# Performance work log

Hardware: AMD Instinct MI355X
Metric: run time of the kernel (lower is better)

The kernel has to match this reference:

```python
import jax, jax.numpy as jnp
import numpy as np

NUM_HEADS = 8
SCALE = 25.0
SIM_THRESH = 0.75


def setup_inputs() -> dict:
    key = jax.random.key(0)
    k1, k2, k3, k4 = jax.random.split(key, 4)
    B, N, C = 1, 2048, 1024
    x_cls = jax.random.normal(k1, (B, N, C), jnp.float32)
    cls_score = jax.random.uniform(k2, (N,), jnp.float32)
    fg_score = jax.random.uniform(k3, (N,), jnp.float32)
    W_qkv = jax.random.normal(k4, (3 * C, C), jnp.float32) * 0.02
    return {"x_cls": x_cls, "cls_score": cls_score, "fg_score": fg_score, "W_qkv": W_qkv}


def reference(x_cls, cls_score, fg_score, W_qkv):
    B, N, C = x_cls.shape
    H = NUM_HEADS
    hd = C // H
    # qkv projection (Linear without bias): [B,N,3C] -> [3,B,H,N,hd]
    qkv = (x_cls @ W_qkv.T).reshape(B, N, 3, H, hd).transpose(2, 0, 3, 1, 4)
    q, k, v = qkv[0], qkv[1], qkv[2]
    # cosine normalization
    qn = q / jnp.linalg.norm(q, axis=-1, keepdims=True)
    kn = k / jnp.linalg.norm(k, axis=-1, keepdims=True)
    vn = v / jnp.linalg.norm(v, axis=-1, keepdims=True)
    # cls_score broadcast to [1,1,1,N] (columns); fg_score is unused downstream
    cs = cls_score.reshape(1, 1, 1, N)
    # raw v-v similarity map [B,H,N,N]
    attn_cls_raw = vn @ jnp.swapaxes(vn, -2, -1)
    # use_mask=True path: mask[i,j] = cls_score[j] > cls_score[i] - 0.1
    cs_mask = (cs > jnp.swapaxes(cs, -2, -1) - 0.1).astype(x_cls.dtype)
    # scaled, score-weighted, masked attention; dropout p=0 is identity
    attn = jax.nn.softmax((qn @ jnp.swapaxes(kn, -2, -1)) * SCALE * cs * cs_mask, axis=-1)
    x = jnp.swapaxes(attn @ v, 1, 2).reshape(B, N, C)
    x_ori = jnp.swapaxes(v, 1, 2).reshape(B, N, C)
    x_out = jnp.concatenate([x, x_ori], axis=-1)  # [B,N,2C]
    # ave=True branch: head-averaged similarity + second softmax, masked renorm
    sim_raw = attn_cls_raw.sum(axis=1)[0] / H  # [N,N]
    sim_mask = (sim_raw > SIM_THRESH).astype(x_cls.dtype)
    sim_attn = attn.sum(axis=1)[0] / H
    sim_round2 = jax.nn.softmax(sim_attn, axis=-1)
    masked = sim_mask * sim_round2
    sim_round2 = masked / jnp.sum(masked, axis=-1, keepdims=True)
    return (x_out, sim_round2)
```

## Files before the change

### kernel.cpp

```cpp
#include <hip/hip_runtime.h>
#include <cstdint>

typedef unsigned short u16;
typedef __attribute__((ext_vector_type(8))) short short8;
typedef __attribute__((ext_vector_type(4))) short short4v;
typedef __attribute__((ext_vector_type(4))) float f32x4;

#define NTOK 2048
#define CDIM 1024
#define C3   3072
#define NH   8
#define HD   128

__device__ __forceinline__ float bf2f(u16 u) {
    return __uint_as_float(((unsigned)u) << 16);
}
__device__ __forceinline__ u16 f2bf(float f) {
    unsigned u = __float_as_uint(f);
    u += 0x7fffu + ((u >> 16) & 1u);
    return (u16)(u >> 16);
}
__device__ __forceinline__ void gld_lds16(const u16* g, u16* l) {
    __builtin_amdgcn_global_load_lds(
        (__attribute__((address_space(1))) void*)(u16*)g,
        (__attribute__((address_space(3))) void*)l, 16, 0, 0);
}

__global__ __launch_bounds__(256) void k_cast(const float* __restrict__ x,
                                              const float* __restrict__ w,
                                              u16* __restrict__ xb,
                                              u16* __restrict__ wb) {
    int t = blockIdx.x * blockDim.x + threadIdx.x;
    int stride = gridDim.x * blockDim.x;
    for (int i = t; i < (NTOK * CDIM) / 4; i += stride) {
        float4 v = ((const float4*)x)[i];
        ushort4 o;
        o.x = f2bf(v.x); o.y = f2bf(v.y); o.z = f2bf(v.z); o.w = f2bf(v.w);
        ((ushort4*)xb)[i] = o;
    }
    for (int i = t; i < (C3 * CDIM) / 4; i += stride) {
        float4 v = ((const float4*)w)[i];
        ushort4 o;
        o.x = f2bf(v.x); o.y = f2bf(v.y); o.z = f2bf(v.z); o.w = f2bf(v.w);
        ((ushort4*)wb)[i] = o;
    }
}

__global__ __launch_bounds__(256) void k_qkvn(const u16* __restrict__ A,
                                              const u16* __restrict__ B,
                                              u16* __restrict__ Qn,
                                              u16* __restrict__ Kn,
                                              u16* __restrict__ Vn,
                                              u16* __restrict__ Vt,
                                              float* __restrict__ out) {
    __shared__ u16 SB[2][16384];
    __shared__ float rowssq[128][2];
    u16* T = (u16*)SB;
    const int tid = threadIdx.x;
    const int lane = tid & 63;
    const int wid = tid >> 6;
    const int wm = wid >> 1, wn = wid & 1;
    const int q = lane >> 4, l16 = lane & 15;
    const int s = blockIdx.x;
    const int which = s >> 3, h = s & 7;
    const int m0 = blockIdx.y * 128, n0 = s * 128;

    const u16* aP[4];
    const u16* bP[4];
#pragma unroll
    for (int t = 0; t < 4; t++) {
        int sl = tid + t * 256;
        int r = sl >> 3, c = (sl & 7) * 8;
        aP[t] = &A[(long long)(m0 + r) * CDIM + c];
        bP[t] = &B[(long long)(n0 + r) * CDIM + c];
    }
#pragma unroll
    for (int t = 0; t < 4; t++) {
        int sl = tid + t * 256;
        gld_lds16(aP[t], &SB[0][sl * 8]);
        gld_lds16(bP[t], &SB[0][8192 + sl * 8]);
        aP[t] += 64;
        bP[t] += 64;
    }

    f32x4 zero4 = {0.f, 0.f, 0.f, 0.f};
    f32x4 acc[4][4];
#pragma unroll
    for (int i = 0; i < 4; i++)
#pragma unroll
        for (int j = 0; j < 4; j++) acc[i][j] = zero4;

    for (int jt = 0; jt < 16; ++jt) {
        const u16* As = SB[jt & 1];
        const u16* Bs = SB[jt & 1] + 8192;
        asm volatile("s_waitcnt vmcnt(0)" ::: "memory");
        __builtin_amdgcn_s_barrier();
        asm volatile("" ::: "memory");
        if (jt < 15) {
            u16* Sx = SB[(jt + 1) & 1];
#pragma unroll
            for (int t = 0; t < 4; t++) {
                int sl = tid + t * 256;
                gld_lds16(aP[t], &Sx[sl * 8]);
                gld_lds16(bP[t], &Sx[8192 + sl * 8]);
                aP[t] += 64;
                bP[t] += 64;
            }
        }
#pragma unroll
        for (int ks = 0; ks < 2; ks++) {
            short8 af[4], bfr[4];
#pragma unroll
            for (int tm = 0; tm < 4; tm++)
                af[tm] = *(const short8*)&As[(wm * 64 + tm * 16 + l16) * 64 + ks * 32 + q * 8];
#pragma unroll
            for (int tn = 0; tn < 4; tn++)
                bfr[tn] = *(const short8*)&Bs[(wn * 64 + tn * 16 + l16) * 64 + ks * 32 + q * 8];
#pragma unroll
            for (int tm = 0; tm < 4; tm++)
#pragma unroll
                for (int tn = 0; tn < 4; tn++)
                    acc[tm][tn] = __builtin_amdgcn_mfma_f32_16x16x32_bf16(
                        af[tm], bfr[tn], acc[tm][tn], 0, 0, 0);
        }
    }

    __syncthreads();
#pragma unroll
    for (int tm = 0; tm < 4; tm++)
#pragma unroll
        for (int r = 0; r < 4; r++) {
            float p = 0.f;
#pragma unroll
            for (int tn = 0; tn < 4; tn++) p += acc[tm][tn][r] * acc[tm][tn][r];
            p += __shfl_xor(p, 1);
            p += __shfl_xor(p, 2);
            p += __shfl_xor(p, 4);
            p += __shfl_xor(p, 8);
            if (l16 == 0) rowssq[wm * 64 + tm * 16 + q * 4 + r][wn] = p;
        }
    __syncthreads();
    float rinv[4][4];
#pragma unroll
    for (int tm = 0; tm < 4; tm++)
#pragma unroll
        for (int r = 0; r < 4; r++) {
            int rl = wm * 64 + tm * 16 + q * 4 + r;
            rinv[tm][r] = rsqrtf(rowssq[rl][0] + rowssq[rl][1]);
        }
    u16* dstBase = (which == 0 ? Qn : which == 1 ? Kn : Vn);
#pragma unroll
    for (int tm = 0; tm < 4; tm++)
#pragma unroll
        for (int tn = 0; tn < 4; tn++)
#pragma unroll
            for (int r = 0; r < 4; r++) {
                int rl = wm * 64 + tm * 16 + q * 4 + r;
                int d = wn * 64 + tn * 16 + l16;
                dstBase[(long long)(m0 + rl) * CDIM + h * HD + d] =
                    f2bf(acc[tm][tn][r] * rinv[tm][r]);
            }
    if (which == 2) {
#pragma unroll
        for (int tm = 0; tm < 4; tm++)
#pragma unroll
            for (int tn = 0; tn < 4; tn++)
#pragma unroll
                for (int r = 0; r < 4; r++) {
                    int rl = wm * 64 + tm * 16 + q * 4 + r;
                    int d = wn * 64 + tn * 16 + l16;
                    float v = acc[tm][tn][r];
                    out[(long long)(m0 + rl) * 2048 + 1024 + h * HD + d] = v;
                    T[rl * 136 + d] = f2bf(v);
                }
        __syncthreads();
#pragma unroll
        for (int p = 0; p < 2; p++) {
            int drow = p * 64 + (tid >> 2);
            int nc = (tid & 3) * 32;
            u16 buf[32];
#pragma unroll
            for (int i = 0; i < 32; i++) buf[i] = T[(nc + i) * 136 + drow];
            u16* dst = &Vt[(long long)(h * HD + drow) * NTOK + m0 + nc];
            *(short8*)&dst[0] = *(short8*)&buf[0];
            *(short8*)&dst[8] = *(short8*)&buf[8];
            *(short8*)&dst[16] = *(short8*)&buf[16];
            *(short8*)&dst[24] = *(short8*)&buf[24];
        }
    }
}

__global__ __launch_bounds__(256) void k_gemm_mask(const u16* __restrict__ A,
                                                   const u16* __restrict__ B,
                                                   unsigned char* __restrict__ Cv,
                                                   int K, int lda, int ldb, int ldc,
                                                   float scale) {
    __shared__ u16 As2[2][8192];
    __shared__ u16 Bs2[2][4096];
    __shared__ __attribute__((aligned(16))) unsigned char Tm[128][80];
    const int tid = threadIdx.x;
    const int lane = tid & 63;
    const int wid = tid >> 6;
    const int wm = wid >> 1, wn = wid & 1;
    const int q = lane >> 4, l16 = lane & 15;
    const int bid = blockIdx.x + 32 * blockIdx.y;
    const int sw = (bid & 7) * 64 + (bid >> 3);
    const int m0 = (sw >> 5) * 128, n0 = (sw & 31) * 64;

    const u16* aP[4];
    const u16* bP[2];
#pragma unroll
    for (int t = 0; t < 4; t++) {
        int s = tid + t * 256;
        aP[t] = &A[(long long)(m0 + (s >> 3)) * lda + (s & 7) * 8];
    }
#pragma unroll
    for (int t = 0; t < 2; t++) {
        int s = tid + t * 256;
        bP[t] = &B[(long long)(n0 + (s >> 3)) * ldb + (s & 7) * 8];
    }
#pragma unroll
    for (int t = 0; t < 4; t++) { gld_lds16(aP[t], &As2[0][(tid + t * 256) * 8]); aP[t] += 64; }
#pragma unroll
    for (int t = 0; t < 2; t++) { gld_lds16(bP[t], &Bs2[0][(tid + t * 256) * 8]); bP[t] += 64; }

    f32x4 zero4 = {0.f, 0.f, 0.f, 0.f};
    f32x4 acc[4][2];
#pragma unroll
    for (int i = 0; i < 4; i++)
#pragma unroll
        for (int j = 0; j < 2; j++) acc[i][j] = zero4;

    const int NIT = K / 64;
    for (int jt = 0; jt < NIT; ++jt) {
        const u16* As = As2[jt & 1];
        const u16* Bs = Bs2[jt & 1];
        asm volatile("s_waitcnt vmcnt(0)" ::: "memory");
        __builtin_amdgcn_s_barrier();
        asm volatile("" ::: "memory");
        if (jt < NIT - 1) {
            u16* Ax = As2[(jt + 1) & 1];
            u16* Bx = Bs2[(jt + 1) & 1];
#pragma unroll
            for (int t = 0; t < 4; t++) { gld_lds16(aP[t], &Ax[(tid + t * 256) * 8]); aP[t] += 64; }
#pragma unroll
            for (int t = 0; t < 2; t++) { gld_lds16(bP[t], &Bx[(tid + t * 256) * 8]); bP[t] += 64; }
        }
#pragma unroll
        for (int ks = 0; ks < 2; ks++) {
            short8 af[4], bfr[2];
#pragma unroll
            for (int tm = 0; tm < 4; tm++)
                af[tm] = *(const short8*)&As[(wm * 64 + tm * 16 + l16) * 64 + ks * 32 + q * 8];
#pragma unroll
            for (int tn = 0; tn < 2; tn++)
                bfr[tn] = *(const short8*)&Bs[(wn * 32 + tn * 16 + l16) * 64 + ks * 32 + q * 8];
#pragma unroll
            for (int tm = 0; tm < 4; tm++)
#pragma unroll
                for (int tn = 0; tn < 2; tn++)
                    acc[tm][tn] = __builtin_amdgcn_mfma_f32_16x16x32_bf16(
                        af[tm], bfr[tn], acc[tm][tn], 0, 0, 0);
        }
    }

#pragma unroll
    for (int tm = 0; tm < 4; tm++)
#pragma unroll
        for (int tn = 0; tn < 2; tn++) {
            int col = wn * 32 + tn * 16 + l16;
            int rowbase = wm * 64 + tm * 16 + q * 4;
#pragma unroll
            for (int r = 0; r < 4; r++)
                Tm[rowbase + r][col] = (acc[tm][tn][r] * scale > 0.75f) ? 1 : 0;
        }
    __syncthreads();
    {
        int row = tid >> 1, half = (tid & 1) * 32;
        const short8* sm = (const short8*)&Tm[row][half];
        short8* dm = (short8*)&Cv[(long long)(m0 + row) * ldc + n0 + half];
        dm[0] = sm[0]; dm[1] = sm[1];
    }
}

__global__ __launch_bounds__(256, 2) void k_attn9(const u16* __restrict__ Qn,
                                                  const u16* __restrict__ Kn,
                                                  const u16* __restrict__ Vt,
                                                  const float* __restrict__ cls,
                                                  u16* __restrict__ P,
                                                  float* __restrict__ Spart,
                                                  u16* __restrict__ Xpart) {
    __shared__ u16 Kf[2][8192];
    __shared__ u16 Vf[2][8192];
    __shared__ u16 Et[8192];
    const int bid = blockIdx.x + 16 * (blockIdx.y + 4 * blockIdx.z);
    const int sw = (bid & 7) * 64 + (bid >> 3);
    const int h = sw >> 6;
    const int jc = (sw >> 4) & 3;
    const int i0 = (sw & 15) * 128;
    const int jbase = jc * 512;
    const int tid = threadIdx.x, lane = tid & 63, wid = tid >> 6;
    const int q = lane >> 4, l16 = lane & 15;
    const int wm = wid >> 1, wn = wid & 1;

    short8 af[4][4];
#pragma unroll
    for (int m = 0; m < 4; m++)
#pragma unroll
        for (int kt = 0; kt < 4; kt++)
            af[m][kt] = *(const short8*)&Qn[(long long)(i0 + wm * 64 + m * 16 + l16) * CDIM +
                                            h * HD + kt * 32 + q * 8];
    float cls_i[4][4];
#pragma unroll
    for (int m = 0; m < 4; m++)
#pragma unroll
        for (int r = 0; r < 4; r++)
            cls_i[m][r] = cls[i0 + wm * 64 + m * 16 + q * 4 + r] - 0.1f;

    const u16* ksrc[4];
    const u16* vsrc[4];
#pragma unroll
    for (int t = 0; t < 4; t++) {
        int g = wid * 4 + t;
        int tn = g >> 2, kt = g & 3;
        ksrc[t] = &Kn[(long long)(jbase + tn * 16 + l16) * CDIM + h * HD + kt * 32 + q * 8];
        int n = g >> 1, ks = g & 1;
        vsrc[t] = &Vt[(long long)(h * HD + n * 16 + l16) * NTOK + jbase + (ks * 4 + q) * 8];
    }

    f32x4 zero4 = {0.f, 0.f, 0.f, 0.f};
    f32x4 pv[4][4];
#pragma unroll
    for (int m = 0; m < 4; m++)
#pragma unroll
        for (int n = 0; n < 4; n++) pv[m][n] = zero4;
    float sums[4][4];
#pragma unroll
    for (int m = 0; m < 4; m++)
#pragma unroll
        for (int r = 0; r < 4; r++) sums[m][r] = 0.f;

#pragma unroll
    for (int t = 0; t < 4; t++) {
        int g = wid * 4 + t;
        gld_lds16(ksrc[t], &Kf[0][(g * 64 + lane) * 8]);
        gld_lds16(vsrc[t], &Vf[0][(g * 64 + lane) * 8]);
        ksrc[t] += 64 * CDIM;
        vsrc[t] += 64;
    }

    for (int jt = 0; jt < 8; ++jt) {
        const int j0 = jbase + jt * 64;
        const int cur = jt & 1;
        u16* Kc = Kf[cur];
        if (jt == 0)
            asm volatile("s_waitcnt vmcnt(0)" ::: "memory");
        else
            asm volatile("s_waitcnt vmcnt(4)" ::: "memory");
        float cjv[2];
        cjv[0] = cls[j0 + (wn * 2 + 0) * 16 + l16];
        cjv[1] = cls[j0 + (wn * 2 + 1) * 16 + l16];
        asm volatile("" ::: "memory");
        __builtin_amdgcn_s_barrier();
        asm volatile("" ::: "memory");
        if (jt < 7) {
            u16* Kx = Kf[cur ^ 1];
            u16* Vx = Vf[cur ^ 1];
#pragma unroll
            for (int t = 0; t < 4; t++) {
                int g = wid * 4 + t;
                gld_lds16(ksrc[t], &Kx[(g * 64 + lane) * 8]);
                gld_lds16(vsrc[t], &Vx[(g * 64 + lane) * 8]);
                ksrc[t] += 64 * CDIM;
                vsrc[t] += 64;
            }
        }
#pragma unroll
        for (int tn = 0; tn < 2; tn++) {
            int tng = wn * 2 + tn;
            short8 bfr[4];
#pragma unroll
            for (int kt = 0; kt < 4; kt++)
                bfr[kt] = *(const short8*)&Kc[((tng * 4 + kt) * 64 + lane) * 8];
            float cj = cjv[tn];
            float sc = 25.f * cj;
#pragma unroll
            for (int m = 0; m < 4; m++) {
                f32x4 acc = zero4;
                __builtin_amdgcn_s_setprio(1);
#pragma unroll
                for (int kt = 0; kt < 4; kt++)
                    acc = __builtin_amdgcn_mfma_f32_16x16x32_bf16(af[m][kt], bfr[kt],
                                                                  acc, 0, 0, 0);
                __builtin_amdgcn_s_setprio(0);
                int ibase = wm * 64 + m * 16 + q * 4;
#pragma unroll
                for (int r = 0; r < 4; r++) {
                    float mk = (cj > cls_i[m][r]) ? 1.f : 0.f;
                    float e = __expf(acc[r] * sc * mk);
                    sums[m][r] += e;
                    int il = ibase + r;
                    int jl = tng * 16 + l16;
                    Et[il * 64 + ((((jl >> 3) ^ (il & 7)) << 3) | (jl & 7))] = f2bf(e);
                }
            }
        }
        asm volatile("s_waitcnt lgkmcnt(0)" ::: "memory");
        __builtin_amdgcn_s_barrier();
        asm volatile("" ::: "memory");
        {
            int il = tid >> 1, c4 = (tid & 1) * 4;
            int x = il & 7;
            short8 e0 = *(const short8*)&Et[il * 64 + (((c4 + 0) ^ x) << 3)];
            short8 e1 = *(const short8*)&Et[il * 64 + (((c4 + 1) ^ x) << 3)];
            short8 e2 = *(const short8*)&Et[il * 64 + (((c4 + 2) ^ x) << 3)];
            short8 e3 = *(const short8*)&Et[il * 64 + (((c4 + 3) ^ x) << 3)];
            u16* dst = &P[((long long)(h * NTOK + i0 + il)) * NTOK + j0 + c4 * 8];
            *(short8*)&dst[0] = e0;
            *(short8*)&dst[8] = e1;
            *(short8*)&dst[16] = e2;
            *(short8*)&dst[24] = e3;
        }
        __builtin_amdgcn_s_setprio(1);
#pragma unroll
        for (int ks = 0; ks < 2; ks++) {
            short8 a2[4];
#pragma unroll
            for (int m2 = 0; m2 < 4; m2++) {
                int il = wm * 64 + m2 * 16 + l16;
                int ch = ks * 4 + q;
                a2[m2] = *(const short8*)&Et[il * 64 + ((ch ^ (il & 7)) << 3)];
            }
#pragma unroll
            for (int n2 = 0; n2 < 4; n2++) {
                short8 b2 = *(const short8*)&Vf[cur][(((wn * 4 + n2) * 2 + ks) * 64 + lane) * 8];
#pragma unroll
                for (int m2 = 0; m2 < 4; m2++)
                    pv[m2][n2] = __builtin_amdgcn_mfma_f32_16x16x32_bf16(
                        a2[m2], b2, pv[m2][n2], 0, 0, 0);
            }
        }
        __builtin_amdgcn_s_setprio(0);
    }
#pragma unroll
    for (int m = 0; m < 4; m++)
#pragma unroll
        for (int r = 0; r < 4; r++) {
            float s = sums[m][r];
            s += __shfl_xor(s, 1);
            s += __shfl_xor(s, 2);
            s += __shfl_xor(s, 4);
            s += __shfl_xor(s, 8);
            if (l16 == 0)
                Spart[((wn * 4 + jc) * NH + h) * NTOK + i0 + wm * 64 + m * 16 + q * 4 + r] = s;
        }
    u16* Xp = Xpart + (long long)jc * NTOK * CDIM;
#pragma unroll
    for (int m2 = 0; m2 < 4; m2++)
#pragma unroll
        for (int n2 = 0; n2 < 4; n2++)
#pragma unroll
            for (int r = 0; r < 4; r++) {
                int i = i0 + wm * 64 + m2 * 16 + q * 4 + r;
                int d = wn * 64 + n2 * 16 + l16;
                Xp[(long long)i * CDIM + h * HD + d] = f2bf(pv[m2][n2][r]);
            }
}

__global__ __launch_bounds__(256) void k_epi(const u16* __restrict__ Xpart,
                                             const float* __restrict__ Spart,
                                             const u16* __restrict__ P,
                                             const unsigned char* __restrict__ mask,
                                             float* __restrict__ out,
                                             float* __restrict__ out2) {
    __shared__ float red[256];
    __shared__ float sArr[NH];
    const int i = blockIdx.x;
    const int t = threadIdx.x;
    if (t < NH) {
        float s = 0.f;
#pragma unroll
        for (int g = 0; g < 8; g++) s += Spart[(g * NH + t) * NTOK + i];
        sArr[t] = s;
    }
    __syncthreads();
    {
        int c = t * 4;
        int h = c >> 7;
        float acc[4] = {0.f, 0.f, 0.f, 0.f};
#pragma unroll
        for (int jc = 0; jc < 4; jc++) {
            short4v v = *(const short4v*)&Xpart[(long long)jc * NTOK * CDIM +
                                                (long long)i * CDIM + c];
#pragma unroll
            for (int k = 0; k < 4; k++) acc[k] += bf2f((u16)v[k]);
        }
        float invs = 1.f / sArr[h];
        float4 o;
        o.x = acc[0] * invs; o.y = acc[1] * invs; o.z = acc[2] * invs; o.w = acc[3] * invs;
        *(float4*)&out[(long long)i * 2048 + c] = o;
    }
    float invS[NH];
#pragma unroll
    for (int h = 0; h < NH; h++) invS[h] = 1.f / (8.f * sArr[h]);
    const int c0 = t * 8;
    float a[8] = {0.f, 0.f, 0.f, 0.f, 0.f, 0.f, 0.f, 0.f};
#pragma unroll
    for (int h = 0; h < NH; h++) {
        short8 p = *(const short8*)&P[((long long)h * NTOK + i) * NTOK + c0];
#pragma unroll
        for (int k = 0; k < 8; k++) a[k] += bf2f((u16)p[k]) * invS[h];
    }
    const unsigned char* mrow = mask + (long long)i * NTOK + c0;
    float e[8];
    unsigned char mk[8];
    float part = 0.f;
#pragma unroll
    for (int k = 0; k < 8; k++) {
        e[k] = __expf(a[k]);
        mk[k] = mrow[k];
        if (mk[k]) part += e[k];
    }
    red[t] = part;
    __syncthreads();
    for (int s = 128; s > 0; s >>= 1) {
        if (t < s) red[t] += red[t + s];
        __syncthreads();
    }
    float invT = 1.f / red[0];
    float o[8];
#pragma unroll
    for (int k = 0; k < 8; k++) o[k] = mk[k] ? e[k] * invT : 0.f;
    float4 o0, o1;
    o0.x = o[0]; o0.y = o[1]; o0.z = o[2]; o0.w = o[3];
    o1.x = o[4]; o1.y = o[5]; o1.z = o[6]; o1.w = o[7];
    float* dst = out2 + (long long)i * NTOK + c0;
    *(float4*)dst = o0;
    *(float4*)(dst + 4) = o1;
}

extern "C" void kernel_launch(void* const* d_in, const int* in_sizes, int n_in,
                              void* d_out, int out_size, void* d_ws,
                              size_t ws_size, hipStream_t stream) {
    (void)in_sizes; (void)n_in; (void)out_size; (void)ws_size;
    const float* x = (const float*)d_in[0];
    const float* cls = (const float*)d_in[1];
    const float* Wq = (const float*)d_in[3];
    float* out = (float*)d_out;
    char* ws = (char*)d_ws;

    u16* Xb = (u16*)(ws + 0);
    u16* Wb = (u16*)(ws + 4194304);
    u16* Xpart = (u16*)(ws + 0);
    float* Spart = (float*)(ws + 16777216);
    u16* Qn = (u16*)(ws + 23068672);
    u16* Kn = (u16*)(ws + 27262976);
    u16* Vn = (u16*)(ws + 31457280);
    u16* Vt = (u16*)(ws + 35651584);
    unsigned char* mask = (unsigned char*)(ws + 39845888);
    u16* P = (u16*)(ws + 44040192);

    k_cast<<<1024, 256, 0, stream>>>(x, Wq, Xb, Wb);

    k_qkvn<<<dim3(24, 16), 256, 0, stream>>>(Xb, Wb, Qn, Kn, Vn, Vt, out);

    k_gemm_mask<<<dim3(32, 16), 256, 0, stream>>>(
        Vn, Vn, mask, CDIM, CDIM, CDIM, NTOK, 0.125f);

    k_attn9<<<dim3(16, 4, NH), 256, 0, stream>>>(Qn, Kn, Vt, cls, P, Spart, Xpart);

    k_epi<<<NTOK, 256, 0, stream>>>(Xpart, Spart, P, mask, out,
                                    out + (long long)NTOK * 2048);
}
```

Before: 196.5 us.

## Halve attention row tile and drop LDS double buffering for higher occupancy

The attention kernel now processes 64 query rows per block instead of 128, so it launches twice as many blocks. It also replaces the double-buffered K/V LDS tiles with a single buffer that is loaded synchronously each iteration. Together these cut LDS and register use so the launch bound can allow 4 blocks per CU, relying on more resident waves to hide latency. The cost is that K/V loads are no longer prefetched during compute, each K/V tile is reloaded by twice as many blocks, and there is an extra barrier per tile.

```diff
diff --git a/kernel.cpp b/kernel.cpp
--- a/kernel.cpp
+++ b/kernel.cpp
@@ -283,39 +283,39 @@
     }
 }
 
-__global__ __launch_bounds__(256, 2) void k_attn9(const u16* __restrict__ Qn,
-                                                  const u16* __restrict__ Kn,
-                                                  const u16* __restrict__ Vt,
-                                                  const float* __restrict__ cls,
-                                                  u16* __restrict__ P,
-                                                  float* __restrict__ Spart,
-                                                  u16* __restrict__ Xpart) {
-    __shared__ u16 Kf[2][8192];
-    __shared__ u16 Vf[2][8192];
-    __shared__ u16 Et[8192];
-    const int bid = blockIdx.x + 16 * (blockIdx.y + 4 * blockIdx.z);
-    const int sw = (bid & 7) * 64 + (bid >> 3);
-    const int h = sw >> 6;
-    const int jc = (sw >> 4) & 3;
-    const int i0 = (sw & 15) * 128;
+__global__ __launch_bounds__(256, 4) void k_attn10(const u16* __restrict__ Qn,
+                                                   const u16* __restrict__ Kn,
+                                                   const u16* __restrict__ Vt,
+                                                   const float* __restrict__ cls,
+                                                   u16* __restrict__ P,
+                                                   float* __restrict__ Spart,
+                                                   u16* __restrict__ Xpart) {
+    __shared__ u16 Kf[8192];
+    __shared__ u16 Vf[8192];
+    __shared__ u16 Et[4096];
+    const int bid = blockIdx.x + 32 * (blockIdx.y + 4 * blockIdx.z);
+    const int sw = (bid & 7) * 128 + (bid >> 3);
+    const int h = sw >> 7;
+    const int jc = (sw >> 5) & 3;
+    const int i0 = (sw & 31) * 64;
     const int jbase = jc * 512;
     const int tid = threadIdx.x, lane = tid & 63, wid = tid >> 6;
     const int q = lane >> 4, l16 = lane & 15;
     const int wm = wid >> 1, wn = wid & 1;
 
-    short8 af[4][4];
-#pragma unroll
-    for (int m = 0; m < 4; m++)
+    short8 af[2][4];
+#pragma unroll
+    for (int m = 0; m < 2; m++)
 #pragma unroll
         for (int kt = 0; kt < 4; kt++)
-            af[m][kt] = *(const short8*)&Qn[(long long)(i0 + wm * 64 + m * 16 + l16) * CDIM +
+            af[m][kt] = *(const short8*)&Qn[(long long)(i0 + wm * 32 + m * 16 + l16) * CDIM +
                                             h * HD + kt * 32 + q * 8];
-    float cls_i[4][4];
-#pragma unroll
-    for (int m = 0; m < 4; m++)
+    float cls_i[2][4];
+#pragma unroll
+    for (int m = 0; m < 2; m++)
 #pragma unroll
         for (int r = 0; r < 4; r++)
-            cls_i[m][r] = cls[i0 + wm * 64 + m * 16 + q * 4 + r] - 0.1f;
+            cls_i[m][r] = cls[i0 + wm * 32 + m * 16 + q * 4 + r] - 0.1f;
 
     const u16* ksrc[4];
     const u16* vsrc[4];
@@ -329,63 +329,44 @@
     }
 
     f32x4 zero4 = {0.f, 0.f, 0.f, 0.f};
-    f32x4 pv[4][4];
-#pragma unroll
-    for (int m = 0; m < 4; m++)
+    f32x4 pv[2][4];
+#pragma unroll
+    for (int m = 0; m < 2; m++)
 #pragma unroll
         for (int n = 0; n < 4; n++) pv[m][n] = zero4;
-    float sums[4][4];
-#pragma unroll
-    for (int m = 0; m < 4; m++)
-#pragma unroll
-        for (int r = 0; r < 4; r++) sums[m][r] = 0.f;
-
-#pragma unroll
-    for (int t = 0; t < 4; t++) {
-        int g = wid * 4 + t;
-        gld_lds16(ksrc[t], &Kf[0][(g * 64 + lane) * 8]);
-        gld_lds16(vsrc[t], &Vf[0][(g * 64 + lane) * 8]);
-        ksrc[t] += 64 * CDIM;
-        vsrc[t] += 64;
-    }
+    float sums[2][4] = {{0.f, 0.f, 0.f, 0.f}, {0.f, 0.f, 0.f, 0.f}};
 
     for (int jt = 0; jt < 8; ++jt) {
         const int j0 = jbase + jt * 64;
-        const int cur = jt & 1;
-        u16* Kc = Kf[cur];
-        if (jt == 0)
-            asm volatile("s_waitcnt vmcnt(0)" ::: "memory");
-        else
-            asm volatile("s_waitcnt vmcnt(4)" ::: "memory");
+        if (jt > 0) {
+            __builtin_amdgcn_s_barrier();
+            asm volatile("" ::: "memory");
+        }
+#pragma unroll
+        for (int t = 0; t < 4; t++) {
+            int g = wid * 4 + t;
+            gld_lds16(ksrc[t], &Kf[(g * 64 + lane) * 8]);
+            gld_lds16(vsrc[t], &Vf[(g * 64 + lane) * 8]);
+            ksrc[t] += 64 * CDIM;
+            vsrc[t] += 64;
+        }
         float cjv[2];
         cjv[0] = cls[j0 + (wn * 2 + 0) * 16 + l16];
         cjv[1] = cls[j0 + (wn * 2 + 1) * 16 + l16];
-        asm volatile("" ::: "memory");
+        asm volatile("s_waitcnt vmcnt(0)" ::: "memory");
         __builtin_amdgcn_s_barrier();
         asm volatile("" ::: "memory");
-        if (jt < 7) {
-            u16* Kx = Kf[cur ^ 1];
-            u16* Vx = Vf[cur ^ 1];
-#pragma unroll
-            for (int t = 0; t < 4; t++) {
-                int g = wid * 4 + t;
-                gld_lds16(ksrc[t], &Kx[(g * 64 + lane) * 8]);
-                gld_lds16(vsrc[t], &Vx[(g * 64 + lane) * 8]);
-                ksrc[t] += 64 * CDIM;
-                vsrc[t] += 64;
-            }
-        }
 #pragma unroll
         for (int tn = 0; tn < 2; tn++) {
             int tng = wn * 2 + tn;
             short8 bfr[4];
 #pragma unroll
             for (int kt = 0; kt < 4; kt++)
-                bfr[kt] = *(const short8*)&Kc[((tng * 4 + kt) * 64 + lane) * 8];
+                bfr[kt] = *(const short8*)&Kf[((tng * 4 + kt) * 64 + lane) * 8];
             float cj = cjv[tn];
             float sc = 25.f * cj;
 #pragma unroll
-            for (int m = 0; m < 4; m++) {
+            for (int m = 0; m < 2; m++) {
                 f32x4 acc = zero4;
                 __builtin_amdgcn_s_setprio(1);
 #pragma unroll
@@ -393,7 +374,7 @@
                     acc = __builtin_amdgcn_mfma_f32_16x16x32_bf16(af[m][kt], bfr[kt],
                                                                   acc, 0, 0, 0);
                 __builtin_amdgcn_s_setprio(0);
-                int ibase = wm * 64 + m * 16 + q * 4;
+                int ibase = wm * 32 + m * 16 + q * 4;
 #pragma unroll
                 for (int r = 0; r < 4; r++) {
                     float mk = (cj > cls_i[m][r]) ? 1.f : 0.f;
@@ -409,33 +390,29 @@
         __builtin_amdgcn_s_barrier();
         asm volatile("" ::: "memory");
         {
-            int il = tid >> 1, c4 = (tid & 1) * 4;
+            int il = tid >> 2, c = tid & 3;
             int x = il & 7;
-            short8 e0 = *(const short8*)&Et[il * 64 + (((c4 + 0) ^ x) << 3)];
-            short8 e1 = *(const short8*)&Et[il * 64 + (((c4 + 1) ^ x) << 3)];
-            short8 e2 = *(const short8*)&Et[il * 64 + (((c4 + 2) ^ x) << 3)];
-            short8 e3 = *(const short8*)&Et[il * 64 + (((c4 + 3) ^ x) << 3)];
-            u16* dst = &P[((long long)(h * NTOK + i0 + il)) * NTOK + j0 + c4 * 8];
+            short8 e0 = *(const short8*)&Et[il * 64 + (((2 * c) ^ x) << 3)];
+            short8 e1 = *(const short8*)&Et[il * 64 + (((2 * c + 1) ^ x) << 3)];
+            u16* dst = &P[((long long)(h * NTOK + i0 + il)) * NTOK + j0 + c * 16];
             *(short8*)&dst[0] = e0;
             *(short8*)&dst[8] = e1;
-            *(short8*)&dst[16] = e2;
-            *(short8*)&dst[24] = e3;
         }
         __builtin_amdgcn_s_setprio(1);
 #pragma unroll
         for (int ks = 0; ks < 2; ks++) {
-            short8 a2[4];
-#pragma unroll
-            for (int m2 = 0; m2 < 4; m2++) {
-                int il = wm * 64 + m2 * 16 + l16;
+            short8 a2[2];
+#pragma unroll
+            for (int m2 = 0; m2 < 2; m2++) {
+                int il = wm * 32 + m2 * 16 + l16;
                 int ch = ks * 4 + q;
                 a2[m2] = *(const short8*)&Et[il * 64 + ((ch ^ (il & 7)) << 3)];
             }
 #pragma unroll
             for (int n2 = 0; n2 < 4; n2++) {
-                short8 b2 = *(const short8*)&Vf[cur][(((wn * 4 + n2) * 2 + ks) * 64 + lane) * 8];
-#pragma unroll
-                for (int m2 = 0; m2 < 4; m2++)
+                short8 b2 = *(const short8*)&Vf[(((wn * 4 + n2) * 2 + ks) * 64 + lane) * 8];
+#pragma unroll
+                for (int m2 = 0; m2 < 2; m2++)
                     pv[m2][n2] = __builtin_amdgcn_mfma_f32_16x16x32_bf16(
                         a2[m2], b2, pv[m2][n2], 0, 0, 0);
             }
@@ -443,7 +420,7 @@
         __builtin_amdgcn_s_setprio(0);
     }
 #pragma unroll
-    for (int m = 0; m < 4; m++)
+    for (int m = 0; m < 2; m++)
 #pragma unroll
         for (int r = 0; r < 4; r++) {
             float s = sums[m][r];
@@ -452,16 +429,16 @@
             s += __shfl_xor(s, 4);
             s += __shfl_xor(s, 8);
             if (l16 == 0)
-                Spart[((wn * 4 + jc) * NH + h) * NTOK + i0 + wm * 64 + m * 16 + q * 4 + r] = s;
+                Spart[((wn * 4 + jc) * NH + h) * NTOK + i0 + wm * 32 + m * 16 + q * 4 + r] = s;
         }
     u16* Xp = Xpart + (long long)jc * NTOK * CDIM;
 #pragma unroll
-    for (int m2 = 0; m2 < 4; m2++)
+    for (int m2 = 0; m2 < 2; m2++)
 #pragma unroll
         for (int n2 = 0; n2 < 4; n2++)
 #pragma unroll
             for (int r = 0; r < 4; r++) {
-                int i = i0 + wm * 64 + m2 * 16 + q * 4 + r;
+                int i = i0 + wm * 32 + m2 * 16 + q * 4 + r;
                 int d = wn * 64 + n2 * 16 + l16;
                 Xp[(long long)i * CDIM + h * HD + d] = f2bf(pv[m2][n2][r]);
             }
@@ -567,7 +544,7 @@
     k_gemm_mask<<<dim3(32, 16), 256, 0, stream>>>(
         Vn, Vn, mask, CDIM, CDIM, CDIM, NTOK, 0.125f);
 
-    k_attn9<<<dim3(16, 4, NH), 256, 0, stream>>>(Qn, Kn, Vt, cls, P, Spart, Xpart);
+    k_attn10<<<dim3(32, 4, NH), 256, 0, stream>>>(Qn, Kn, Vt, cls, P, Spart, Xpart);
 
     k_epi<<<NTOK, 256, 0, stream>>>(Xpart, Spart, P, mask, out,
                                     out + (long long)NTOK * 2048);
```

After: 248.9 us. +26.6%, slower.
